# Performance work log

Measured on AMD Instinct MI355X. Metric: run time of the kernel, lower is better.

## Reference

```python
import jax, jax.numpy as jnp
import numpy as np

# dims
B, N, L = 8, 128, 512          # batch, n_vars, context_window
PL, ST = 16, 8                  # patch_len, stride
PN = (L - PL) // ST + 1         # patch_num = 63
DM, H, DFF, NL = 128, 16, 256, 2
DK = DM // H
DG, MP, BETA = 8, 3, 0.05       # d_gcn, mp_layers, propbeta
TW = 96                         # target_window


def setup_inputs() -> dict:
    key = jax.random.key(0)
    ks = iter(jax.random.split(key, 64))
    def nrm(shape, s=0.02):
        return jax.random.normal(next(ks), shape, jnp.float32) * s
    inp = {
        "x": jax.random.normal(next(ks), (B, N, L), jnp.float32),
        "adj_logits": jax.random.normal(next(ks), (B, L, N, N), jnp.float32),
        # DGCN params
        "dgcn_start_w": nrm((1, DG)), "dgcn_start_b": jnp.zeros((DG,), jnp.float32),
        "dgcn_mlp_w": nrm(((MP + 1) * DG, 1)), "dgcn_mlp_b": jnp.zeros((1,), jnp.float32),
        # patch embedding + positional
        "W_P": nrm((PL, DM)), "b_P": jnp.zeros((DM,), jnp.float32), "W_pos": nrm((PN, DM)),
        # encoder layers (stacked over NL)
        "Wq": nrm((NL, DM, DM)), "bq": jnp.zeros((NL, DM), jnp.float32),
        "Wk": nrm((NL, DM, DM)), "bk": jnp.zeros((NL, DM), jnp.float32),
        "Wv": nrm((NL, DM, DM)), "bv": jnp.zeros((NL, DM), jnp.float32),
        "Wo": nrm((NL, DM, DM)), "bo": jnp.zeros((NL, DM), jnp.float32),
        "scale": jnp.full((NL,), DK ** -0.5, jnp.float32),
        "bn1_g": jnp.ones((NL, DM), jnp.float32), "bn1_b": jnp.zeros((NL, DM), jnp.float32),
        "ff_w1": nrm((NL, DM, DFF)), "ff_b1": jnp.zeros((NL, DFF), jnp.float32),
        "ff_w2": nrm((NL, DFF, DM)), "ff_b2": jnp.zeros((NL, DM), jnp.float32),
        "bn2_g": jnp.ones((NL, DM), jnp.float32), "bn2_b": jnp.zeros((NL, DM), jnp.float32),
        # head
        "head_w": nrm((DM * PN, TW)), "head_b": jnp.zeros((TW,), jnp.float32),
    }
    return inp


def _bn(x, g, b):
    # BatchNorm1d in training mode over (batch, seq) per feature channel
    mu = x.mean(axis=(0, 1))
    var = x.var(axis=(0, 1))
    return (x - mu) * jax.lax.rsqrt(var + 1e-5) * g + b


def reference(x, adj_logits, dgcn_start_w, dgcn_start_b, dgcn_mlp_w, dgcn_mlp_b,
              W_P, b_P, W_pos, Wq, bq, Wk, bk, Wv, bv, Wo, bo, scale,
              bn1_g, bn1_b, ff_w1, ff_b1, ff_w2, ff_b2, bn2_g, bn2_b,
              head_w, head_b):
    # ---- DGCN: multi-hop diffusion over variables, per time step ----
    x4 = x[..., None]                                   # [b,n,s,1]
    A = jax.nn.softmax(adj_logits, axis=2)              # [b,s,n,m], normalized over source n
    a = jnp.transpose(A, (0, 2, 3, 1))                  # [b,n,m,s]
    h = x4 @ dgcn_start_w + dgcn_start_b                # [b,n,s,d_gcn]
    outs = [h]
    for _ in range(MP):
        h = BETA * x4 + (1.0 - BETA) * jnp.einsum('bnsc,bnms->bmsc', h, a)
        outs.append(h)
    y = (jnp.concatenate(outs, axis=-1) @ dgcn_mlp_w + dgcn_mlp_b)[..., 0]  # [b,n,s]
    # ---- patching ----
    win = jnp.arange(PN)[:, None] * ST + jnp.arange(PL)[None, :]
    z = y[:, :, win]                                    # [b,n,pn,pl]
    # ---- TSTiEncoder (channel independent) ----
    src = (z @ W_P + b_P).reshape(B * N, PN, DM) + W_pos
    prev = None
    for l in range(NL):
        q = (src @ Wq[l] + bq[l]).reshape(-1, PN, H, DK).transpose(0, 2, 1, 3)
        k = (src @ Wk[l] + bk[l]).reshape(-1, PN, H, DK).transpose(0, 2, 1, 3)
        v = (src @ Wv[l] + bv[l]).reshape(-1, PN, H, DK).transpose(0, 2, 1, 3)
        scores = jnp.einsum('bhqd,bhkd->bhqk', q, k) * scale[l]
        if prev is not None:
            scores = scores + prev                      # residual attention
        w = jax.nn.softmax(scores, axis=-1)
        o = jnp.einsum('bhqk,bhkd->bhqd', w, v).transpose(0, 2, 1, 3).reshape(-1, PN, DM)
        src = _bn(src + (o @ Wo[l] + bo[l]), bn1_g[l], bn1_b[l])
        ff = jax.nn.gelu(src @ ff_w1[l] + ff_b1[l], approximate=False) @ ff_w2[l] + ff_b2[l]
        src = _bn(src + ff, bn2_g[l], bn2_b[l])
        prev = scores
    # ---- Flatten_Head ----
    enc = src.reshape(B, N, PN, DM).transpose(0, 1, 3, 2).reshape(B, N, DM * PN)
    return enc @ head_w + head_b                        # [b, n_vars, target_window]
```

## Files before the change

### kernel.cpp

```cpp
#include <hip/hip_runtime.h>
#include <hip/hip_bf16.h>
#include <math.h>

#define RM 64512

typedef short short8 __attribute__((ext_vector_type(8)));
typedef float f32x4 __attribute__((ext_vector_type(4)));
typedef unsigned short ushort4v __attribute__((ext_vector_type(4)));
typedef unsigned short ushort8v __attribute__((ext_vector_type(8)));

__device__ __forceinline__ float gelu_f(float v) {
    return 0.5f * v * (1.0f + erff(v * 0.70710678118654752f));
}
__device__ __forceinline__ float b2f(unsigned short u) {
    unsigned int x = ((unsigned int)u) << 16;
    return __builtin_bit_cast(float, x);
}
__device__ __forceinline__ unsigned short f2b(float f) {
    __hip_bfloat16 h = __float2bfloat16(f);
    return __builtin_bit_cast(unsigned short, h);
}

__global__ __launch_bounds__(256) void wprep_kernel(
    const float* __restrict__ Wq, const float* __restrict__ Wk, const float* __restrict__ Wv,
    const float* __restrict__ Wo, const float* __restrict__ fw1, const float* __restrict__ fw2,
    const float* __restrict__ bq, const float* __restrict__ bk, const float* __restrict__ bv,
    unsigned short* __restrict__ WB, float* __restrict__ bcat)
{
    const int id = blockIdx.y;
    const int l = id / 6, mat = id % 6;
    const float* src; int K, N; size_t off = (size_t)l * 131072;
    switch (mat) {
        case 0: src = Wq  + l*16384; K = 128; N = 128; off += 0;      break;
        case 1: src = Wk  + l*16384; K = 128; N = 128; off += 16384;  break;
        case 2: src = Wv  + l*16384; K = 128; N = 128; off += 32768;  break;
        case 3: src = Wo  + l*16384; K = 128; N = 128; off += 49152;  break;
        case 4: src = fw1 + l*32768; K = 128; N = 256; off += 65536;  break;
        default:src = fw2 + l*32768; K = 256; N = 128; off += 98304;  break;
    }
    const int total = K * N;
    const int ksh = (K == 256) ? 8 : 7;
    for (int idx = blockIdx.x*256 + threadIdx.x; idx < total; idx += gridDim.x*256) {
        int n = idx >> ksh, k = idx & (K - 1);
        WB[off + idx] = f2b(src[(size_t)k*N + n]);
    }
    if (id == 0 && blockIdx.x == 0) {
        for (int idx = threadIdx.x; idx < 768; idx += 256) {
            int ll = idx / 384, j = idx % 384;
            float vv;
            if (j < 128)      vv = bq[ll*128 + j];
            else if (j < 256) vv = bk[ll*128 + j - 128];
            else              vv = bv[ll*128 + j - 256];
            bcat[idx] = vv;
        }
    }
}

__global__ __launch_bounds__(256) void dgcn_kernel(
    const float* __restrict__ x, const float* __restrict__ adj,
    const float* __restrict__ sw, const float* __restrict__ sb,
    const float* __restrict__ mw, const float* __restrict__ mb,
    float* __restrict__ y)
{
    __shared__ __align__(16) unsigned short ET[128*128];
    __shared__ __align__(16) unsigned short hT[16*128];
    __shared__ float red[256];
    __shared__ float iv[128];
    __shared__ float xc[128];
    __shared__ float yac[128];
    const int bid = blockIdx.x;
    const int b = bid >> 9, s = bid & 511;
    const int t = threadIdx.x;
    const int lane = t & 63, wid = t >> 6;
    const float* ap = adj + (size_t)bid * 16384;

    if (t < 128) xc[t] = x[((size_t)b*128 + t)*512 + s];

    {
        const int m = t & 127, ng = t >> 7;
        float sm = 0.f;
        for (int p = 0; p < 16; ++p) {
            const int n0 = p*8 + ng*4;
            float e0 = __expf(ap[(size_t)(n0+0)*128 + m]);
            float e1 = __expf(ap[(size_t)(n0+1)*128 + m]);
            float e2 = __expf(ap[(size_t)(n0+2)*128 + m]);
            float e3 = __expf(ap[(size_t)(n0+3)*128 + m]);
            sm += e0 + e1 + e2 + e3;
            ushort4v u4; u4[0]=f2b(e0); u4[1]=f2b(e1); u4[2]=f2b(e2); u4[3]=f2b(e3);
            *(ushort4v*)((char*)ET + m*256 + (((n0>>3) ^ (m & 15))*16) + (n0 & 7)*2) = u4;
        }
        red[ng*128 + m] = sm;
        *(ushort4v*)&hT[8*128 + t*4] = (ushort4v){0,0,0,0};
    }
    __syncthreads();
    if (t < 128) iv[t] = 1.f / (red[t] + red[128 + t]);
    if (t < 128) {
        const int m = t;
        const float xm = xc[m];
        float yp = 0.f;
        #pragma unroll
        for (int c = 0; c < 8; ++c) {
            float h = xm*sw[c] + sb[c];
            yp += h*mw[c];
            *(unsigned short*)((char*)hT + c*256 + ((((m>>3) ^ c))*16) + (m & 7)*2) = f2b(h);
        }
        yac[m] = yp;
    }
    __syncthreads();

    const int rl = lane & 15, kh = lane >> 4;
    short8 af[2][4];
    float xr[2][4], ivr[2][4];
    #pragma unroll
    for (int ti = 0; ti < 2; ++ti) {
        const int mrow = (wid*2 + ti)*16 + rl;
        #pragma unroll
        for (int ks = 0; ks < 4; ++ks) {
            const int ch = (ks*4 + kh) ^ (mrow & 15);
            af[ti][ks] = *(const short8*)((const char*)ET + mrow*256 + ch*16);
        }
        #pragma unroll
        for (int r = 0; r < 4; ++r) {
            const int m = (wid*2 + ti)*16 + kh*4 + r;
            xr[ti][r]  = 0.05f * xc[m];
            ivr[ti][r] = 0.95f * iv[m];
        }
    }
    float yl[2][4] = {};
    #pragma unroll
    for (int step = 1; step <= 3; ++step) {
        short8 bfr[4];
        #pragma unroll
        for (int ks = 0; ks < 4; ++ks) {
            const int ch = (ks*4 + kh) ^ rl;
            bfr[ks] = *(const short8*)((const char*)hT + rl*256 + ch*16);
        }
        f32x4 acc[2] = {};
        #pragma unroll
        for (int ti = 0; ti < 2; ++ti)
            #pragma unroll
            for (int ks = 0; ks < 4; ++ks)
                acc[ti] = __builtin_amdgcn_mfma_f32_16x16x32_bf16(af[ti][ks], bfr[ks], acc[ti], 0, 0, 0);
        __syncthreads();
        const float mwc = (rl < 8) ? mw[step*8 + rl] : 0.f;
        #pragma unroll
        for (int ti = 0; ti < 2; ++ti) {
            const int m0 = (wid*2 + ti)*16 + kh*4;
            ushort4v hw4;
            float hnew[4];
            #pragma unroll
            for (int r = 0; r < 4; ++r) {
                float v = xr[ti][r] + ivr[ti][r]*acc[ti][r];
                hnew[r] = v;
                hw4[r] = f2b(v);
            }
            *(ushort4v*)((char*)hT + rl*256 + (((m0>>3) ^ rl)*16) + (m0 & 7)*2) = hw4;
            #pragma unroll
            for (int r = 0; r < 4; ++r) {
                float vv = hnew[r]*mwc;
                vv += __shfl_xor(vv, 1);
                vv += __shfl_xor(vv, 2);
                vv += __shfl_xor(vv, 4);
                vv += __shfl_xor(vv, 8);
                yl[ti][r] += vv;
            }
        }
        __syncthreads();
    }
    if (rl == 0) {
        #pragma unroll
        for (int ti = 0; ti < 2; ++ti)
            #pragma unroll
            for (int r = 0; r < 4; ++r)
                yac[(wid*2 + ti)*16 + kh*4 + r] += yl[ti][r];
    }
    __syncthreads();
    if (t < 128) y[((size_t)b*128 + t)*512 + s] = yac[t] + mb[0];
}

__global__ __launch_bounds__(256) void patch_kernel(
    const float* __restrict__ y, const float* __restrict__ Wp, const float* __restrict__ bp,
    const float* __restrict__ Wpos, unsigned short* __restrict__ srcb)
{
    __shared__ float ys[512];
    __shared__ float wps[16*128];
    const int bn = blockIdx.x;
    const int t = threadIdx.x;
    ys[t]       = y[(size_t)bn*512 + t];
    ys[t + 256] = y[(size_t)bn*512 + t + 256];
    #pragma unroll
    for (int r = 0; r < 8; ++r) wps[t + r*256] = Wp[t + r*256];
    __syncthreads();
    for (int cu = t; cu < 1008; cu += 256) {
        int p = cu >> 4, d0 = (cu & 15) * 8;
        float o[8];
        #pragma unroll
        for (int j = 0; j < 8; ++j) o[j] = bp[d0+j] + Wpos[p*128 + d0 + j];
        #pragma unroll
        for (int tt = 0; tt < 16; ++tt) {
            float a = ys[p*8 + tt];
            #pragma unroll
            for (int j = 0; j < 8; ++j) o[j] += a * wps[tt*128 + d0 + j];
        }
        size_t row = (size_t)bn*63 + p;
        ushort8v u;
        #pragma unroll
        for (int j = 0; j < 8; ++j) u[j] = f2b(o[j]);
        *(ushort8v*)&srcb[row*128 + d0] = u;
    }
}

template<int ACT, int OM, int RESMODE, bool STATS, bool AHM, int NB, int KK>
__global__ __launch_bounds__(256) void mgemm(
    const unsigned short* __restrict__ A, const unsigned short* __restrict__ WB,
    const float* __restrict__ bias, const unsigned short* __restrict__ Rsd,
    const float* __restrict__ snR,
    unsigned short* __restrict__ Cb,
    float* __restrict__ part)
{
    constexpr int NTOT = NB * 128;
    constexpr int kch = KK >> 3;
    constexpr int KT = KK >> 7;
    __shared__ __align__(16) unsigned short AsL[128*128];
    __shared__ __align__(16) unsigned short BsL[128*128];
    __shared__ float sred[4][16][8], qred[4][16][8];
    const int t = threadIdx.x;
    const int lane = t & 63, wid = t >> 6;
    const int wr = wid >> 1, wc = wid & 1;
    const int m0 = blockIdx.x * 128;
    const int kh = lane >> 4, rl = lane & 15;
    float sj[8] = {}, qj[8] = {};

    for (int ib = 0; ib < NB; ++ib) {
        f32x4 acc[4][4] = {};
        for (int kt = 0; kt < KT; ++kt) {
            if (ib == 0 || KT > 1) {
                #pragma unroll
                for (int i = 0; i < 8; ++i) {
                    int cid = i*256 + t;
                    const unsigned short* ga;
                    if constexpr (AHM) {
                        int hd2 = cid >> 7, row = cid & 127;
                        ga = A + ((size_t)hd2*RM + (m0+row))*8;
                    } else {
                        int row = cid >> 4, c = cid & 15;
                        int c_g = c ^ (row & 7);
                        ga = A + ((size_t)(m0+row)*kch + kt*16 + c_g)*8;
                    }
                    __builtin_amdgcn_global_load_lds((const unsigned int*)ga,
                        (unsigned int*)&AsL[(i*256 + wid*64)*8], 16, 0, 0);
                }
            }
            #pragma unroll
            for (int i = 0; i < 8; ++i) {
                int cid = i*256 + t;
                int nr = cid >> 4, c = cid & 15;
                const unsigned short* gb = WB + (size_t)ib*128*KK
                    + ((size_t)nr*kch + kt*16 + (c ^ (nr & 7)))*8;
                __builtin_amdgcn_global_load_lds((const unsigned int*)gb,
                    (unsigned int*)&BsL[(i*256 + wid*64)*8], 16, 0, 0);
            }
            __syncthreads();
            #pragma unroll
            for (int ks = 0; ks < 4; ++ks) {
                const int cA = ks*4 + kh;
                short8 af[4], bfr[4];
                #pragma unroll
                for (int i = 0; i < 4; ++i) {
                    int row = wr*64 + i*16 + rl;
                    if constexpr (AHM) af[i] = *(const short8*)&AsL[(cA*128 + row)*8];
                    else               af[i] = *(const short8*)&AsL[row*128 + ((cA ^ (row & 7))*8)];
                    int cn  = wc*64 + i*16 + rl;
                    bfr[i] = *(const short8*)&BsL[cn*128 + ((cA ^ (cn & 7))*8)];
                }
                #pragma unroll
                for (int i = 0; i < 4; ++i)
                    #pragma unroll
                    for (int j = 0; j < 4; ++j)
                        acc[i][j] = __builtin_amdgcn_mfma_f32_16x16x32_bf16(af[i], bfr[j], acc[i][j], 0, 0, 0);
            }
            __syncthreads();
        }
        #pragma unroll
        for (int j = 0; j < 4; ++j) {
            const int col_l = wc*64 + j*16 + rl;
            const float bs = bias[ib*128 + col_l];
            const int chunk = col_l >> 3, bo2 = (col_l & 7) << 1;
            #pragma unroll
            for (int i = 0; i < 4; ++i) {
                #pragma unroll
                for (int r = 0; r < 4; ++r) {
                    const int row_l = wr*64 + i*16 + (lane>>4)*4 + r;
                    float v = acc[i][j][r] + bs;
                    if constexpr (ACT == 1) v = gelu_f(v);
                    *(unsigned short*)((char*)BsL + row_l*256 + ((chunk ^ (row_l & 15))<<4) + bo2) = f2b(v);
                }
            }
        }
        __syncthreads();
        if constexpr (OM == 1) {
            #pragma unroll
            for (int it = 0; it < 8; ++it) {
                int cid = it*256 + t;
                int row_l = cid & 127, hd_l = cid >> 7;
                ushort8v u = *(const ushort8v*)((const char*)BsL + row_l*256 + ((hd_l ^ (row_l & 15))<<4));
                *(ushort8v*)&Cb[(((size_t)(ib*16 + hd_l))*RM + m0 + row_l)*8] = u;
            }
        } else {
            #pragma unroll
            for (int it = 0; it < 8; ++it) {
                const int row_l = it*16 + (t >> 4), c = t & 15;
                ushort8v u = *(const ushort8v*)((const char*)BsL + row_l*256 + ((c ^ (row_l & 15))<<4));
                const size_t gbase = (size_t)(m0 + row_l)*NTOT + ib*128 + c*8;
                ushort8v rs = {};
                if constexpr (RESMODE != 0) rs = *(const ushort8v*)&Rsd[gbase];
                ushort8v o8;
                #pragma unroll
                for (int jj = 0; jj < 8; ++jj) {
                    float v = b2f(u[jj]);
                    if constexpr (RESMODE == 1) v += b2f(rs[jj]);
                    if constexpr (RESMODE == 2) v += b2f(rs[jj])*snR[c*8+jj] + snR[128 + c*8 + jj];
                    if constexpr (STATS) { sj[jj] += v; qj[jj] += v*v; }
                    o8[jj] = f2b(v);
                }
                *(ushort8v*)&Cb[gbase] = o8;
            }
        }
        __syncthreads();
    }
    if constexpr (STATS) {
        #pragma unroll
        for (int jj = 0; jj < 8; ++jj) {
            sj[jj] += __shfl_xor(sj[jj], 16); qj[jj] += __shfl_xor(qj[jj], 16);
            sj[jj] += __shfl_xor(sj[jj], 32); qj[jj] += __shfl_xor(qj[jj], 32);
        }
        if ((lane >> 4) == 0) {
            #pragma unroll
            for (int jj = 0; jj < 8; ++jj) {
                sred[wid][lane][jj] = sj[jj];
                qred[wid][lane][jj] = qj[jj];
            }
        }
        __syncthreads();
        if (t < 128) {
            const int c2 = t >> 3, jj = t & 7;
            float s = sred[0][c2][jj] + sred[1][c2][jj] + sred[2][c2][jj] + sred[3][c2][jj];
            float q = qred[0][c2][jj] + qred[1][c2][jj] + qred[2][c2][jj] + qred[3][c2][jj];
            part[(size_t)blockIdx.x*256 + t]       = s;
            part[(size_t)blockIdx.x*256 + 128 + t] = q;
        }
    }
}

__global__ __launch_bounds__(256) void bnred(const float* __restrict__ part,
    const float* __restrict__ g, const float* __restrict__ b, float* __restrict__ sn)
{
    const int c = blockIdx.x, t = threadIdx.x;
    float s = 0.f, q = 0.f;
    for (int bid = t; bid < 504; bid += 256) {
        s += part[(size_t)bid*256 + c];
        q += part[(size_t)bid*256 + 128 + c];
    }
    __shared__ float ls[256], lq[256];
    ls[t] = s; lq[t] = q;
    __syncthreads();
    for (int o = 128; o > 0; o >>= 1) {
        if (t < o) { ls[t] += ls[t+o]; lq[t] += lq[t+o]; }
        __syncthreads();
    }
    if (t == 0) {
        const float invM = 1.f / (float)RM;
        float mean = ls[0] * invM;
        float var  = fmaxf(lq[0]*invM - mean*mean, 0.f);
        float sc = g[c] * rsqrtf(var + 1e-5f);
        sn[c]       = sc;
        sn[128 + c] = b[c] - mean*sc;
    }
}

__global__ __launch_bounds__(256) void wfold(const unsigned short* __restrict__ WBs,
    const float* __restrict__ sn, const float* __restrict__ bsrc,
    unsigned short* __restrict__ WBd, float* __restrict__ bdst)
{
    const int t = threadIdx.x, wv = t >> 6, lane = t & 63;
    const int n = blockIdx.x*4 + wv;
    float w1 = b2f(WBs[(size_t)n*128 + lane]);
    float w2 = b2f(WBs[(size_t)n*128 + 64 + lane]);
    WBd[(size_t)n*128 + lane]      = f2b(sn[lane]*w1);
    WBd[(size_t)n*128 + 64 + lane] = f2b(sn[64+lane]*w2);
    float bacc = sn[128+lane]*w1 + sn[192+lane]*w2;
    #pragma unroll
    for (int msk = 1; msk < 64; msk <<= 1) bacc += __shfl_xor(bacc, msk);
    if (lane == 0) bdst[n] = bsrc[n] + bacc;
}

__global__ __launch_bounds__(256) void attn_kernel(
    const unsigned short* __restrict__ qkv, const unsigned short* __restrict__ qkvP,
    const float* __restrict__ scale, const int l, unsigned short* __restrict__ ob)
{
    __shared__ float ks[4][504], vs[4][504], k0s[4][504];
    const int bn = blockIdx.x;
    const int t = threadIdx.x, wid = t >> 6, lane = t & 63;
    const int hd = blockIdx.y*4 + wid;
    const size_t rbase = (size_t)hd*RM + (size_t)bn*63;
    float qr[8] = {}, q0r[8] = {};
    if (lane < 63) {
        ushort8v ku = *(const ushort8v*)&qkv[((size_t)16*RM*8) + (rbase + lane)*8];
        ushort8v vu = *(const ushort8v*)&qkv[((size_t)32*RM*8) + (rbase + lane)*8];
        #pragma unroll
        for (int d = 0; d < 8; ++d) { ks[wid][lane*8+d] = b2f(ku[d]); vs[wid][lane*8+d] = b2f(vu[d]); }
        ushort8v qu = *(const ushort8v*)&qkv[(rbase + lane)*8];
        #pragma unroll
        for (int d = 0; d < 8; ++d) qr[d] = b2f(qu[d]);
        if (l > 0) {
            ushort8v k0u = *(const ushort8v*)&qkvP[((size_t)16*RM*8) + (rbase + lane)*8];
            #pragma unroll
            for (int d = 0; d < 8; ++d) k0s[wid][lane*8+d] = b2f(k0u[d]);
            ushort8v q0u = *(const ushort8v*)&qkvP[(rbase + lane)*8];
            #pragma unroll
            for (int d = 0; d < 8; ++d) q0r[d] = b2f(q0u[d]);
        }
    }
    __syncthreads();
    if (lane >= 63) return;
    const float scl  = scale[l];
    const float scl0 = (l > 0) ? scale[0] : 0.f;
    float mr = 0.f, sum = 0.f;
    float oa[8] = {};
    for (int j = 0; j < 63; ++j) {
        float s = 0.f;
        #pragma unroll
        for (int d = 0; d < 8; ++d) s += qr[d]*ks[wid][j*8+d];
        s *= scl;
        if (l > 0) {
            float s0 = 0.f;
            #pragma unroll
            for (int d = 0; d < 8; ++d) s0 += q0r[d]*k0s[wid][j*8+d];
            s += scl0 * s0;
        }
        if (j == 0) {
            mr = s; sum = 1.f;
            #pragma unroll
            for (int d = 0; d < 8; ++d) oa[d] = vs[wid][d];
        } else if (s > mr + 8.f) {
            float c = __expf(mr - s);
            sum = sum*c + 1.f;
            #pragma unroll
            for (int d = 0; d < 8; ++d) oa[d] = oa[d]*c + vs[wid][j*8+d];
            mr = s;
        } else {
            float p = __expf(s - mr);
            sum += p;
            #pragma unroll
            for (int d = 0; d < 8; ++d) oa[d] += p*vs[wid][j*8+d];
        }
    }
    float inv = 1.f / sum;
    ushort8v u;
    #pragma unroll
    for (int d = 0; d < 8; ++d) u[d] = f2b(oa[d]*inv);
    *(ushort8v*)&ob[((size_t)hd*RM + (size_t)bn*63 + lane)*8] = u;
}

__global__ __launch_bounds__(256) void hwfold(
    const float* __restrict__ hw, const float* __restrict__ hb,
    const float* __restrict__ sn,
    unsigned short* __restrict__ hwTf, float* __restrict__ hbf)
{
    const int n = blockIdx.x;
    const int t = threadIdx.x;
    float bacc = 0.f;
    if (n < 96) {
        for (int idx = t; idx < 8192; idx += 256) {
            int ksv = idx >> 8, kl = idx & 255;
            unsigned short w = 0;
            if (kl < 252) {
                int k = ksv*252 + kl;
                int d = (int)(((unsigned)k * 33289u) >> 21);
                float wv = hw[(size_t)k*96 + n];
                w = f2b(sn[d] * wv);
                bacc += sn[128 + d] * wv;
            }
            hwTf[(size_t)(ksv*128 + n)*256 + kl] = w;
        }
    } else {
        for (int idx = t; idx < 8192; idx += 256) {
            int ksv = idx >> 8, kl = idx & 255;
            hwTf[(size_t)(ksv*128 + n)*256 + kl] = 0;
        }
    }
    __shared__ float ls[256];
    ls[t] = bacc;
    __syncthreads();
    for (int o = 128; o > 0; o >>= 1) { if (t < o) ls[t] += ls[t+o]; __syncthreads(); }
    if (t == 0 && n < 96) hbf[n] = hb[n] + ls[0];
}

__global__ __launch_bounds__(256) void mhead(
    const unsigned short* __restrict__ A, const unsigned short* __restrict__ BW,
    float* __restrict__ part)
{
    __shared__ __align__(16) unsigned short AsL[128*128];
    __shared__ __align__(16) unsigned short BsL[128*128];
    const int t = threadIdx.x;
    const int lane = t & 63, wid = t >> 6;
    const int wr = wid >> 1, wc = wid & 1;
    const int m0 = blockIdx.x * 128;
    const int ks = blockIdx.y;
    f32x4 acc[4][3] = {};
    for (int kt = 0; kt < 2; ++kt) {
        #pragma unroll
        for (int i = 0; i < 8; ++i) {
            int cid = i*256 + t;
            int nr = cid >> 4, c = cid & 15;
            const unsigned short* gb = BW + ((size_t)(ks*128 + nr)*256 + kt*128 + ((c ^ (nr & 7))*8));
            __builtin_amdgcn_global_load_lds((const unsigned int*)gb,
                (unsigned int*)&BsL[(i*256 + wid*64)*8], 16, 0, 0);
        }
        #pragma unroll
        for (int i = 0; i < 8; ++i) {
            int cid = i*256 + t;
            int row = cid >> 4, c_lds = cid & 15;
            int c_g = c_lds ^ (row & 7);
            int kl0 = kt*128 + c_g*8;
            ushort8v u;
            #pragma unroll
            for (int j = 0; j < 8; ++j) {
                int kl = kl0 + j;
                if (kl < 252) {
                    int dl = (kl*521) >> 15;
                    int p  = kl - dl*63;
                    u[j] = A[((size_t)(m0+row)*63 + p)*128 + ks*4 + dl];
                } else u[j] = 0;
            }
            *(ushort8v*)&AsL[cid*8] = u;
        }
        __syncthreads();
        const int kh = lane >> 4, rl = lane & 15;
        #pragma unroll
        for (int kq = 0; kq < 4; ++kq) {
            const int cA = kq*4 + kh;
            short8 af[4], bfr[3];
            #pragma unroll
            for (int i = 0; i < 4; ++i) {
                int row = wr*64 + i*16 + rl;
                af[i] = *(const short8*)&AsL[row*128 + ((cA ^ (row & 7))*8)];
            }
            #pragma unroll
            for (int j = 0; j < 3; ++j) {
                int cn = wc*48 + j*16 + rl;
                bfr[j] = *(const short8*)&BsL[cn*128 + ((cA ^ (cn & 7))*8)];
            }
            #pragma unroll
            for (int i = 0; i < 4; ++i)
                #pragma unroll
                for (int j = 0; j < 3; ++j)
                    acc[i][j] = __builtin_amdgcn_mfma_f32_16x16x32_bf16(af[i], bfr[j], acc[i][j], 0, 0, 0);
        }
        __syncthreads();
    }
    const int rl = lane & 15, rq = lane >> 4;
    #pragma unroll
    for (int j = 0; j < 3; ++j) {
        const int col = wc*48 + j*16 + rl;
        #pragma unroll
        for (int i = 0; i < 4; ++i) {
            const int rbase = m0 + wr*64 + i*16 + rq*4;
            #pragma unroll
            for (int r = 0; r < 4; ++r)
                part[((size_t)ks*1024 + rbase + r)*96 + col] = acc[i][j][r];
        }
    }
}

__global__ __launch_bounds__(256) void head_reduce(const float* __restrict__ part,
    const float* __restrict__ hbf, float* __restrict__ out)
{
    int idx = blockIdx.x*256 + threadIdx.x;
    float s = hbf[idx % 96];
    #pragma unroll
    for (int blk = 0; blk < 32; ++blk) s += part[(size_t)blk*98304 + idx];
    out[idx] = s;
}

extern "C" void kernel_launch(void* const* d_in, const int* in_sizes, int n_in,
                              void* d_out, int out_size, void* d_ws, size_t ws_size,
                              hipStream_t stream) {
    const float* x    = (const float*)d_in[0];
    const float* adj  = (const float*)d_in[1];
    const float* sw   = (const float*)d_in[2];
    const float* sb   = (const float*)d_in[3];
    const float* mw   = (const float*)d_in[4];
    const float* mb   = (const float*)d_in[5];
    const float* Wp   = (const float*)d_in[6];
    const float* bp   = (const float*)d_in[7];
    const float* Wpos = (const float*)d_in[8];
    const float* Wq   = (const float*)d_in[9];
    const float* bq   = (const float*)d_in[10];
    const float* Wk   = (const float*)d_in[11];
    const float* bk   = (const float*)d_in[12];
    const float* Wv   = (const float*)d_in[13];
    const float* bv   = (const float*)d_in[14];
    const float* Wo   = (const float*)d_in[15];
    const float* bo   = (const float*)d_in[16];
    const float* scale= (const float*)d_in[17];
    const float* bn1g = (const float*)d_in[18];
    const float* bn1b = (const float*)d_in[19];
    const float* fw1  = (const float*)d_in[20];
    const float* fb1  = (const float*)d_in[21];
    const float* fw2  = (const float*)d_in[22];
    const float* fb2  = (const float*)d_in[23];
    const float* bn2g = (const float*)d_in[24];
    const float* bn2b = (const float*)d_in[25];
    const float* hw   = (const float*)d_in[26];
    const float* hb   = (const float*)d_in[27];
    float* out = (float*)d_out;

    float* y     = (float*)d_ws;
    float* part  = y     + 524288;
    float* snorm = part  + 129024;
    float* bcat  = snorm + 1024;
    float* bfold = bcat  + 768;
    float* hbf   = bfold + 1024;
    float* hpart = hbf   + 128;
    unsigned short* srcb = (unsigned short*)(hpart + 3145728);
    unsigned short* t1b  = srcb + 8257536;
    unsigned short* t2b  = t1b  + 8257536;
    unsigned short* g    = t2b  + 8257536;
    unsigned short* o_bf = g    + 16515072;
    unsigned short* qkv0 = o_bf + 8257536;
    unsigned short* qkv1 = qkv0 + 24772608;
    unsigned short* WB   = qkv1 + 24772608;
    unsigned short* WF   = WB   + 262144;
    unsigned short* hwTf = WF   + 131072;

    wprep_kernel<<<dim3(64,12), 256, 0, stream>>>(Wq, Wk, Wv, Wo, fw1, fw2, bq, bk, bv, WB, bcat);
    dgcn_kernel<<<4096, 256, 0, stream>>>(x, adj, sw, sb, mw, mb, y);
    patch_kernel<<<1024, 256, 0, stream>>>(y, Wp, bp, Wpos, srcb);

    mgemm<0,1,0,false,false,3,128><<<504, 256, 0, stream>>>(srcb, WB, bcat, nullptr, nullptr, qkv0, nullptr);
    attn_kernel<<<dim3(1024,4), 256, 0, stream>>>(qkv0, qkv0, scale, 0, o_bf);
    mgemm<0,2,1,true,true,1,128><<<504, 256, 0, stream>>>(o_bf, WB + 49152, bo, srcb, nullptr, t1b, part);
    bnred<<<128, 256, 0, stream>>>(part, bn1g, bn1b, snorm);
    wfold<<<64, 256, 0, stream>>>(WB + 65536, snorm, fb1, WF, bfold);
    mgemm<1,2,0,false,false,2,128><<<504, 256, 0, stream>>>(t1b, WF, bfold, nullptr, nullptr, g, nullptr);
    mgemm<0,2,2,true,false,1,256><<<504, 256, 0, stream>>>(g, WB + 98304, fb2, t1b, snorm, t2b, part);
    bnred<<<128, 256, 0, stream>>>(part, bn2g, bn2b, snorm + 256);
    wfold<<<96, 256, 0, stream>>>(WB + 131072, snorm + 256, bcat + 384, WF + 65536, bfold + 512);

    mgemm<0,1,0,false,false,3,128><<<504, 256, 0, stream>>>(t2b, WF + 65536, bfold + 512, nullptr, nullptr, qkv1, nullptr);
    attn_kernel<<<dim3(1024,4), 256, 0, stream>>>(qkv1, qkv0, scale, 1, o_bf);
    mgemm<0,2,2,true,true,1,128><<<504, 256, 0, stream>>>(o_bf, WB + 131072 + 49152, bo + 128, t2b, snorm + 256, t1b, part);
    bnred<<<128, 256, 0, stream>>>(part, bn1g + 128, bn1b + 128, snorm + 512);
    wfold<<<64, 256, 0, stream>>>(WB + 131072 + 65536, snorm + 512, fb1 + 256, WF + 32768, bfold + 256);
    mgemm<1,2,0,false,false,2,128><<<504, 256, 0, stream>>>(t1b, WF + 32768, bfold + 256, nullptr, nullptr, g, nullptr);
    mgemm<0,2,2,true,false,1,256><<<504, 256, 0, stream>>>(g, WB + 131072 + 98304, fb2 + 128, t1b, snorm + 512, t2b, part);
    bnred<<<128, 256, 0, stream>>>(part, bn2g + 128, bn2b + 128, snorm + 768);

    hwfold<<<128, 256, 0, stream>>>(hw, hb, snorm + 768, hwTf, hbf);
    mhead<<<dim3(8,32), 256, 0, stream>>>(t2b, hwTf, hpart);
    head_reduce<<<384, 256, 0, stream>>>(hpart, hbf, out);
}
```

Measured before the change: 425.5 us.

## Split head GEMM K by patch so A tiles load contiguously via LDS DMA

The head GEMM's K split changes from 32 chunks of 252 interleaved (d,p) elements to 63 chunks, one per patch position, each covering all 128 model dims. Each A tile then becomes a contiguous 128x128 bf16 block that can be fetched with global_load_lds, replacing the scattered per-element gather with index arithmetic. The folded head weights are re-laid out per patch and the bias fold moves to its own kernel. The cost is more split-K partials (63 instead of 32), a larger workspace, and a heavier reduction pass.

```diff
diff --git a/kernel.cpp b/kernel.cpp
--- a/kernel.cpp
+++ b/kernel.cpp
@@ -463,37 +463,35 @@
 }
 
 __global__ __launch_bounds__(256) void hwfold(
+    const float* __restrict__ hw, const float* __restrict__ sn,
+    unsigned short* __restrict__ hwTf)
+{
+    const int p = blockIdx.x;
+    const int t = threadIdx.x;
+    for (int idx = t; idx < 16384; idx += 256) {
+        int n = idx >> 7, d = idx & 127;
+        unsigned short w = 0;
+        if (n < 96) w = f2b(sn[d] * hw[(size_t)(d*63 + p)*96 + n]);
+        hwTf[((size_t)p*128 + n)*128 + d] = w;
+    }
+}
+
+__global__ __launch_bounds__(256) void hbias(
     const float* __restrict__ hw, const float* __restrict__ hb,
-    const float* __restrict__ sn,
-    unsigned short* __restrict__ hwTf, float* __restrict__ hbf)
+    const float* __restrict__ sn, float* __restrict__ hbf)
 {
     const int n = blockIdx.x;
     const int t = threadIdx.x;
-    float bacc = 0.f;
-    if (n < 96) {
-        for (int idx = t; idx < 8192; idx += 256) {
-            int ksv = idx >> 8, kl = idx & 255;
-            unsigned short w = 0;
-            if (kl < 252) {
-                int k = ksv*252 + kl;
-                int d = (int)(((unsigned)k * 33289u) >> 21);
-                float wv = hw[(size_t)k*96 + n];
-                w = f2b(sn[d] * wv);
-                bacc += sn[128 + d] * wv;
-            }
-            hwTf[(size_t)(ksv*128 + n)*256 + kl] = w;
-        }
-    } else {
-        for (int idx = t; idx < 8192; idx += 256) {
-            int ksv = idx >> 8, kl = idx & 255;
-            hwTf[(size_t)(ksv*128 + n)*256 + kl] = 0;
-        }
+    float acc = 0.f;
+    for (int k = t; k < 8064; k += 256) {
+        int d = (int)(((unsigned)k * 33289u) >> 21);
+        acc += sn[128 + d] * hw[(size_t)k*96 + n];
     }
     __shared__ float ls[256];
-    ls[t] = bacc;
+    ls[t] = acc;
     __syncthreads();
     for (int o = 128; o > 0; o >>= 1) { if (t < o) ls[t] += ls[t+o]; __syncthreads(); }
-    if (t == 0 && n < 96) hbf[n] = hb[n] + ls[0];
+    if (t == 0) hbf[n] = hb[n] + ls[0];
 }
 
 __global__ __launch_bounds__(256) void mhead(
@@ -506,69 +504,56 @@
     const int lane = t & 63, wid = t >> 6;
     const int wr = wid >> 1, wc = wid & 1;
     const int m0 = blockIdx.x * 128;
-    const int ks = blockIdx.y;
+    const int p  = blockIdx.y;
+    #pragma unroll
+    for (int i = 0; i < 8; ++i) {
+        int cid = i*256 + t;
+        int row = cid >> 4, c = cid & 15;
+        const unsigned short* ga = A + ((size_t)(m0+row)*63 + p)*128 + ((c ^ (row & 7))*8);
+        __builtin_amdgcn_global_load_lds((const unsigned int*)ga,
+            (unsigned int*)&AsL[(i*256 + wid*64)*8], 16, 0, 0);
+    }
+    #pragma unroll
+    for (int i = 0; i < 8; ++i) {
+        int cid = i*256 + t;
+        int nr = cid >> 4, c = cid & 15;
+        const unsigned short* gb = BW + ((size_t)p*128 + nr)*128 + ((c ^ (nr & 7))*8);
+        __builtin_amdgcn_global_load_lds((const unsigned int*)gb,
+            (unsigned int*)&BsL[(i*256 + wid*64)*8], 16, 0, 0);
+    }
+    __syncthreads();
+    const int kh = lane >> 4, rl = lane & 15;
     f32x4 acc[4][3] = {};
-    for (int kt = 0; kt < 2; ++kt) {
-        #pragma unroll
-        for (int i = 0; i < 8; ++i) {
-            int cid = i*256 + t;
-            int nr = cid >> 4, c = cid & 15;
-            const unsigned short* gb = BW + ((size_t)(ks*128 + nr)*256 + kt*128 + ((c ^ (nr & 7))*8));
-            __builtin_amdgcn_global_load_lds((const unsigned int*)gb,
-                (unsigned int*)&BsL[(i*256 + wid*64)*8], 16, 0, 0);
-        }
-        #pragma unroll
-        for (int i = 0; i < 8; ++i) {
-            int cid = i*256 + t;
-            int row = cid >> 4, c_lds = cid & 15;
-            int c_g = c_lds ^ (row & 7);
-            int kl0 = kt*128 + c_g*8;
-            ushort8v u;
-            #pragma unroll
-            for (int j = 0; j < 8; ++j) {
-                int kl = kl0 + j;
-                if (kl < 252) {
-                    int dl = (kl*521) >> 15;
-                    int p  = kl - dl*63;
-                    u[j] = A[((size_t)(m0+row)*63 + p)*128 + ks*4 + dl];
-                } else u[j] = 0;
-            }
-            *(ushort8v*)&AsL[cid*8] = u;
-        }
-        __syncthreads();
-        const int kh = lane >> 4, rl = lane & 15;
-        #pragma unroll
-        for (int kq = 0; kq < 4; ++kq) {
-            const int cA = kq*4 + kh;
-            short8 af[4], bfr[3];
-            #pragma unroll
-            for (int i = 0; i < 4; ++i) {
-                int row = wr*64 + i*16 + rl;
-                af[i] = *(const short8*)&AsL[row*128 + ((cA ^ (row & 7))*8)];
-            }
-            #pragma unroll
-            for (int j = 0; j < 3; ++j) {
-                int cn = wc*48 + j*16 + rl;
-                bfr[j] = *(const short8*)&BsL[cn*128 + ((cA ^ (cn & 7))*8)];
-            }
-            #pragma unroll
-            for (int i = 0; i < 4; ++i)
-                #pragma unroll
-                for (int j = 0; j < 3; ++j)
-                    acc[i][j] = __builtin_amdgcn_mfma_f32_16x16x32_bf16(af[i], bfr[j], acc[i][j], 0, 0, 0);
-        }
-        __syncthreads();
-    }
-    const int rl = lane & 15, rq = lane >> 4;
+    #pragma unroll
+    for (int kq = 0; kq < 4; ++kq) {
+        const int cA = kq*4 + kh;
+        short8 af[4], bfr[3];
+        #pragma unroll
+        for (int i = 0; i < 4; ++i) {
+            int row = wr*64 + i*16 + rl;
+            af[i] = *(const short8*)&AsL[row*128 + ((cA ^ (row & 7))*8)];
+        }
+        #pragma unroll
+        for (int j = 0; j < 3; ++j) {
+            int cn = wc*48 + j*16 + rl;
+            bfr[j] = *(const short8*)&BsL[cn*128 + ((cA ^ (cn & 7))*8)];
+        }
+        #pragma unroll
+        for (int i = 0; i < 4; ++i)
+            #pragma unroll
+            for (int j = 0; j < 3; ++j)
+                acc[i][j] = __builtin_amdgcn_mfma_f32_16x16x32_bf16(af[i], bfr[j], acc[i][j], 0, 0, 0);
+    }
+    const int rl2 = lane & 15, rq = lane >> 4;
     #pragma unroll
     for (int j = 0; j < 3; ++j) {
-        const int col = wc*48 + j*16 + rl;
+        const int col = wc*48 + j*16 + rl2;
         #pragma unroll
         for (int i = 0; i < 4; ++i) {
             const int rbase = m0 + wr*64 + i*16 + rq*4;
             #pragma unroll
             for (int r = 0; r < 4; ++r)
-                part[((size_t)ks*1024 + rbase + r)*96 + col] = acc[i][j][r];
+                part[((size_t)p*1024 + rbase + r)*96 + col] = acc[i][j][r];
         }
     }
 }
@@ -579,7 +564,7 @@
     int idx = blockIdx.x*256 + threadIdx.x;
     float s = hbf[idx % 96];
     #pragma unroll
-    for (int blk = 0; blk < 32; ++blk) s += part[(size_t)blk*98304 + idx];
+    for (int blk = 0; blk < 63; ++blk) s += part[(size_t)blk*98304 + idx];
     out[idx] = s;
 }
 
@@ -623,7 +608,7 @@
     float* bfold = bcat  + 768;
     float* hbf   = bfold + 1024;
     float* hpart = hbf   + 128;
-    unsigned short* srcb = (unsigned short*)(hpart + 3145728);
+    unsigned short* srcb = (unsigned short*)(hpart + 6193152);
     unsigned short* t1b  = srcb + 8257536;
     unsigned short* t2b  = t1b  + 8257536;
     unsigned short* g    = t2b  + 8257536;
@@ -657,7 +642,8 @@
     mgemm<0,2,2,true,false,1,256><<<504, 256, 0, stream>>>(g, WB + 131072 + 98304, fb2 + 128, t1b, snorm + 512, t2b, part);
     bnred<<<128, 256, 0, stream>>>(part, bn2g + 128, bn2b + 128, snorm + 768);
 
-    hwfold<<<128, 256, 0, stream>>>(hw, hb, snorm + 768, hwTf, hbf);
-    mhead<<<dim3(8,32), 256, 0, stream>>>(t2b, hwTf, hpart);
+    hwfold<<<63, 256, 0, stream>>>(hw, snorm + 768, hwTf);
+    hbias<<<96, 256, 0, stream>>>(hw, hb, snorm + 768, hbf);
+    mhead<<<dim3(8,63), 256, 0, stream>>>(t2b, hwTf, hpart);
     head_reduce<<<384, 256, 0, stream>>>(hpart, hbf, out);
 }
```

Result: no change. 425.8 us (+0.1%).
